# Kernel optimization log

Measured on AMD Instinct MI355X. Metric: run time of the kernel, lower is better.

The kernel has to match this reference:

```python
import jax, jax.numpy as jnp
import numpy as np

N_QUBITS = 8
N_CYCLES = 4
N_LAYERS = 2  # log2(8) - 1
B = 65536

CNOT = jnp.array([[1, 0, 0, 0],
                  [0, 1, 0, 0],
                  [0, 0, 0, 1],
                  [0, 0, 1, 0]], dtype=jnp.complex64)


def apply_gate(state, U, wires):
    """Apply a (2^k x 2^k) gate U on the given wires of state (B, 2,2,...,2).
    Wire 0 is the leftmost (most significant) qubit axis."""
    k = len(wires)
    src = [w + 1 for w in wires]
    dst = list(range(1, 1 + k))
    st = jnp.moveaxis(state, src, dst)
    shp = st.shape
    st = st.reshape(shp[0], 2 ** k, -1)
    st = jnp.einsum('ij,bjr->bir', U, st)
    return jnp.moveaxis(st.reshape(shp), dst, src)


def apply_ry(state, q, angles):
    """Batched RY(angle) on qubit q; angles has shape (B,)."""
    st = jnp.moveaxis(state, q + 1, 1)  # (B, 2, rest...)
    c = jnp.cos(0.5 * angles).reshape((-1,) + (1,) * (st.ndim - 2))
    s = jnp.sin(0.5 * angles).reshape((-1,) + (1,) * (st.ndim - 2))
    s0, s1 = st[:, 0], st[:, 1]
    new = jnp.stack([c * s0 - s * s1, s * s0 + c * s1], axis=1)
    return jnp.moveaxis(new, 1, q + 1)


def crx_mat(theta):
    c = (jnp.cos(0.5 * theta) + 0j).astype(jnp.complex64)
    s = (-1j * jnp.sin(0.5 * theta)).astype(jnp.complex64)
    one = jnp.ones((), jnp.complex64)
    zero = jnp.zeros((), jnp.complex64)
    return jnp.stack([
        jnp.stack([one, zero, zero, zero]),
        jnp.stack([zero, one, zero, zero]),
        jnp.stack([zero, zero, c, s]),
        jnp.stack([zero, zero, s, c]),
    ])


def u3_mat(p):
    th, ph, lm = p[0], p[1], p[2]
    ct = (jnp.cos(0.5 * th) + 0j).astype(jnp.complex64)
    st = (jnp.sin(0.5 * th) + 0j).astype(jnp.complex64)
    el = jnp.exp(1j * lm).astype(jnp.complex64)
    ep = jnp.exp(1j * ph).astype(jnp.complex64)
    return jnp.stack([
        jnp.stack([ct, -el * st]),
        jnp.stack([ep * st, ep * el * ct]),
    ])


def expval_z(state, q):
    st = jnp.moveaxis(state, q + 1, 1)
    p = (st.real ** 2 + st.imag ** 2).reshape(st.shape[0], 2, -1).sum(-1)
    return p[:, 0] - p[:, 1]


def _forward(x, crx_theta, u3_params, w1, b1, w2, b2):
    b = x.shape[0]
    # |0...0> initial state, shape (B, 2,2,...,2)
    state = jnp.zeros((b, 2 ** N_QUBITS), jnp.complex64).at[:, 0].set(1.0)
    state = state.reshape((b,) + (2,) * N_QUBITS)
    # encoder: data re-uploading RY angle encoding + CNOT ring, n_cycles times
    for _ in range(N_CYCLES):
        for q in range(N_QUBITS):
            state = apply_ry(state, q, x[:, q])
        for q in range(N_QUBITS):
            state = apply_gate(state, CNOT, [q, (q + 1) % N_QUBITS])
    # QCNN conv/pool layers with shared weights per layer
    active = list(range(N_QUBITS))
    for layer in range(N_LAYERS):
        U = crx_mat(crx_theta[layer])
        for i in range(0, len(active) - 1, 2):
            state = apply_gate(state, U, [active[i], active[i + 1]])
        for i in range(1, len(active) - 1, 2):
            state = apply_gate(state, U, [active[i], active[i + 1]])
        remain = active[1::2]
        # mid-circuit expval in the original is discarded and does not alter state
        V = u3_mat(u3_params[layer])
        for q in remain:
            state = apply_gate(state, V, [q])
        active = remain
    feats = jnp.stack([expval_z(state, q) for q in active], axis=1)  # (B, 2)
    h = jnp.tanh(feats @ w1 + b1)
    return jax.nn.sigmoid(h @ w2 + b2)  # (B, 1)


def setup_inputs() -> dict:
    key = jax.random.key(0)
    ks = jax.random.split(key, 6)
    return {
        'x': jax.random.normal(ks[0], (B, N_QUBITS), jnp.float32),
        'crx_theta': jax.random.normal(ks[1], (N_LAYERS,), jnp.float32),
        'u3_params': jax.random.normal(ks[2], (N_LAYERS, 3), jnp.float32),
        'w1': jax.random.normal(ks[3], (2, 10), jnp.float32) * 0.5,
        'b1': jnp.zeros((10,), jnp.float32),
        'w2': jax.random.normal(ks[4], (10, 1), jnp.float32) * 0.5,
        'b2': jnp.zeros((1,), jnp.float32),
    }


def reference(x, crx_theta, u3_params, w1, b1, w2, b2):
    return _forward(x, crx_theta, u3_params, w1, b1, w2, b2)
```

## Files before the change

kernel.cpp:

```cpp
#include <hip/hip_runtime.h>


#define NQ 8
#define NE 2
#define FRAG_OFF 0
#define UR_OFF   65536
#define UI_OFF   98304

typedef _Float16 h2 __attribute__((ext_vector_type(2)));
typedef _Float16 h8 __attribute__((ext_vector_type(8)));
typedef float    f4 __attribute__((ext_vector_type(4)));

__device__ __forceinline__ float h2f(h2 v){ return __builtin_bit_cast(float, v); }
__device__ __forceinline__ h2 f2h(float v){ return __builtin_bit_cast(h2, v); }
__device__ __forceinline__ h2 u2h(unsigned u){ return __builtin_bit_cast(h2, u); }
__device__ __forceinline__ unsigned h2u(h2 v){ return __builtin_bit_cast(unsigned, v); }
__device__ __forceinline__ h2 negh(h2 v){ return u2h(h2u(v) ^ 0x80008000u); }
__device__ __forceinline__ h2 mk(float x){ return __builtin_bit_cast(h2, __builtin_amdgcn_cvt_pkrtz(x,x)); }
__device__ __forceinline__ h2 mk2(float a, float b){ return __builtin_bit_cast(h2, __builtin_amdgcn_cvt_pkrtz(a,b)); }
__device__ __forceinline__ h2 fma2h(h2 a, h2 b, h2 c){ return __builtin_elementwise_fma(a,b,c); }
__device__ __forceinline__ h2 swp(h2 v){ return __builtin_shufflevector(v,v,1,0); }

template<int CTRL>
__device__ __forceinline__ float dppf(float v){
    return __int_as_float(__builtin_amdgcn_mov_dpp(__float_as_int(v), CTRL, 0xF, 0xF, true));
}
template<int M>
__device__ __forceinline__ float sx(float v){
    if constexpr (M==1)       return dppf<0xB1>(v);
    else if constexpr (M==2)  return dppf<0x4E>(v);
    else if constexpr (M==32) return __shfl_xor(v, 32, 64);
    else return __int_as_float(__builtin_amdgcn_ds_swizzle(__float_as_int(v), (M<<10)|0x1F));
}
__device__ __forceinline__ void cmulh(h2&R, h2&I, h2 C, h2 S, h2 nS){
    h2 nR = fma2h(C, R, nS*I);
    I = fma2h(C, I, S*R);
    R = nR;
}

#define FOR_E _Pragma("unroll") for (int e = 0; e < NE; ++e)

#define RINGF() do { FOR_E { \
    h2 TA = pb ? B[e] : A[e]; \
    h2 TS = pb ? A[e] : B[e]; \
    int V0 = (int)__builtin_amdgcn_perm(h2u(TS), h2u(TA), 0x07060100u); \
    int V1 = (int)__builtin_amdgcn_perm(h2u(TA), h2u(TS), 0x07060100u); \
    unsigned r0 = (unsigned)__builtin_amdgcn_ds_bpermute(ba0, V0); \
    unsigned r1 = (unsigned)__builtin_amdgcn_ds_bpermute(ba1, V1); \
    A[e] = u2h(__builtin_amdgcn_perm(r1, r0, 0x07060100u)); \
    B[e] = u2h(__builtin_amdgcn_perm(r1, r0, 0x05040302u)); } \
} while(0)

struct P2C {
    h2 cc0,sn0,nsn0, cc1,sn1,nsn1;
    h2 uct0,ust0,nust0,usv0;
    h2 uct1,ust1,nust1;
    h2 cl1,sl1,nsl1, cp1,sp1,nsp1;
    h2 E0,E1,E2,E3,G2,G3;
    h2 Clm,Slm,nSlm,Cph,Sph,nSph;
    h2 tu1,tu3,tu5;
};

__device__ __forceinline__ P2C load_consts(const unsigned* wsu, int l){
    P2C K;
    const bool L4=(l>>4)&1, L2=(l>>2)&1, L0=l&1;
    K.cc0=u2h(wsu[0]); K.sn0=u2h(wsu[1]); K.cc1=u2h(wsu[2]); K.sn1=u2h(wsu[3]);
    K.nsn0=negh(K.sn0); K.nsn1=negh(K.sn1);
    K.uct0=u2h(wsu[4]); K.ust0=u2h(wsu[5]); K.nust0=u2h(wsu[6]); K.usv0=u2h(wsu[7]);
    K.uct1=u2h(wsu[8]); K.ust1=u2h(wsu[9]); K.nust1=u2h(wsu[10]);
    K.cl1=u2h(wsu[11]); K.sl1=u2h(wsu[12]); K.nsl1=negh(K.sl1);
    K.cp1=u2h(wsu[13]); K.sp1=u2h(wsu[14]); K.nsp1=negh(K.sp1);
    K.E0=u2h(wsu[15]); K.E1=u2h(wsu[16]); K.E2=u2h(wsu[17]);
    K.E3=u2h(wsu[18]); K.G2=u2h(wsu[19]); K.G3=u2h(wsu[20]);
    const int ki = (int)L4 + (int)L2 + (int)L0;
    K.Clm=u2h(wsu[24+ki*4+0]); K.Slm=u2h(wsu[24+ki*4+1]);
    K.Cph=u2h(wsu[24+ki*4+2]); K.Sph=u2h(wsu[24+ki*4+3]);
    K.nSlm=negh(K.Slm); K.nSph=negh(K.Sph);
    K.tu1 = L4 ? K.ust0 : K.nust0;
    K.tu3 = L2 ? K.ust0 : K.nust0;
    K.tu5 = L0 ? K.ust0 : K.nust0;
    return K;
}

#define SHF4(M) h2 oRA[NE], oIA[NE], oRB[NE], oIB[NE]; \
    FOR_E { oRA[e]=f2h(sx<M>(h2f(RA[e]))); oIA[e]=f2h(sx<M>(h2f(IA[e]))); \
            oRB[e]=f2h(sx<M>(h2f(RB[e]))); oIB[e]=f2h(sx<M>(h2f(IB[e]))); }
#define CRX_LL(CSH, M, cc, sn, nsn) do { \
    const bool ct = (l >> (CSH)) & 1; \
    SHF4(M) \
    if (ct) { FOR_E { \
        RA[e] = fma2h(cc, RA[e], (sn)*oIA[e]); IA[e] = fma2h(cc, IA[e], (nsn)*oRA[e]); \
        RB[e] = fma2h(cc, RB[e], (sn)*oIB[e]); IB[e] = fma2h(cc, IB[e], (nsn)*oRB[e]); } } \
} while(0)
#define RYC0(M, T) do { \
    SHF4(M) \
    FOR_E { \
    RA[e] = fma2h(K.uct0, RA[e], (T)*oRA[e]); IA[e] = fma2h(K.uct0, IA[e], (T)*oIA[e]); \
    RB[e] = fma2h(K.uct0, RB[e], (T)*oRB[e]); IB[e] = fma2h(K.uct0, IB[e], (T)*oIB[e]); } \
} while(0)

__device__ __forceinline__ void phase2run(const int l, const P2C& K,
    const h2* A, const h2* B, h2* RA, h2* RB, h2* IA, h2* IB)
{
    const bool L5=(l>>5)&1, L2=(l>>2)&1, L0=l&1;
    FOR_E { RA[e]=A[e]; RB[e]=B[e]; IA[e]=(h2){0,0}; IB[e]=(h2){0,0}; }

    {   h2 oA[NE], oB[NE];
        FOR_E { oA[e]=f2h(sx<16>(h2f(RA[e]))); oB[e]=f2h(sx<16>(h2f(RB[e]))); }
        if (L5){ FOR_E {
            IA[e] = K.nsn0*oA[e]; RA[e] = K.cc0*RA[e];
            IB[e] = K.nsn0*oB[e]; RB[e] = K.cc0*RB[e]; } }
    }
    CRX_LL(3, 4, K.cc0, K.sn0, K.nsn0);
    CRX_LL(1, 1, K.cc0, K.sn0, K.nsn0);
    FOR_E {
        h2 oI = swp(IB[e]), oR = swp(RB[e]);
        RB[e] = fma2h(K.cc0, RB[e], K.sn0*oI);
        IB[e] = fma2h(K.cc0, IB[e], K.nsn0*oR);
    }
    CRX_LL(4, 8, K.cc0, K.sn0, K.nsn0);
    CRX_LL(2, 2, K.cc0, K.sn0, K.nsn0);
    if (L0) { FOR_E {
        h2 nRA = fma2h(K.cc0, RA[e], K.sn0*IB[e]);
        h2 nRB = fma2h(K.cc0, RB[e], K.sn0*IA[e]);
        h2 nIA = fma2h(K.cc0, IA[e], K.nsn0*RB[e]);
        h2 nIB = fma2h(K.cc0, IB[e], K.nsn0*RA[e]);
        RA[e]=nRA; RB[e]=nRB; IA[e]=nIA; IB[e]=nIB; } }
    FOR_E { cmulh(RA[e],IA[e],K.Clm,K.Slm,K.nSlm); cmulh(RB[e],IB[e],K.Clm,K.Slm,K.nSlm); }
    RYC0(16, K.tu1);
    RYC0(4,  K.tu3);
    RYC0(1,  K.tu5);
    FOR_E {
        h2 sA=swp(RA[e]), sB=swp(RB[e]), tA=swp(IA[e]), tB=swp(IB[e]);
        RA[e] = fma2h(K.uct0, RA[e], K.usv0*sA); RB[e] = fma2h(K.uct0, RB[e], K.usv0*sB);
        IA[e] = fma2h(K.uct0, IA[e], K.usv0*tA); IB[e] = fma2h(K.uct0, IB[e], K.usv0*tB);
    }
    FOR_E { cmulh(RA[e],IA[e],K.Cph,K.Sph,K.nSph); cmulh(RB[e],IB[e],K.Cph,K.Sph,K.nSph); }

    CRX_LL(4, 4, K.cc1, K.sn1, K.nsn1);
    if (L0) { FOR_E {
        h2 sIA=swp(IA[e]), sRA=swp(RA[e]), sIB=swp(IB[e]), sRB=swp(RB[e]);
        RA[e] = fma2h(K.cc1, RA[e], K.sn1*sIA); IA[e] = fma2h(K.cc1, IA[e], K.nsn1*sRA);
        RB[e] = fma2h(K.cc1, RB[e], K.sn1*sIB); IB[e] = fma2h(K.cc1, IB[e], K.nsn1*sRB); } }
    CRX_LL(2, 1, K.cc1, K.sn1, K.nsn1);
    {
        if (L2){ FOR_E { cmulh(RA[e],IA[e],K.cl1,K.sl1,K.nsl1); cmulh(RB[e],IB[e],K.cl1,K.sl1,K.nsl1); } }
        h2 T = L2 ? K.ust1 : K.nust1;
        SHF4(4)
        FOR_E {
            RA[e] = fma2h(K.uct1, RA[e], T*oRA[e]); IA[e] = fma2h(K.uct1, IA[e], T*oIA[e]);
            RB[e] = fma2h(K.uct1, RB[e], T*oRB[e]); IB[e] = fma2h(K.uct1, IB[e], T*oIB[e]);
        }
        if (L2){ FOR_E { cmulh(RA[e],IA[e],K.cp1,K.sp1,K.nsp1); cmulh(RB[e],IB[e],K.cp1,K.sp1,K.nsp1); } }
    }
    FOR_E {
        h2 sR=swp(RA[e]), sI=swp(IA[e]);
        h2 nR = fma2h(K.E3,sI, fma2h(K.E2,IA[e], fma2h(K.E1,sR, K.E0*RA[e])));
        h2 nI = fma2h(K.G3,sR, fma2h(K.G2,RA[e], fma2h(K.E1,sI, K.E0*IA[e])));
        RA[e]=nR; IA[e]=nI;
        h2 sR2=swp(RB[e]), sI2=swp(IB[e]);
        h2 nR2 = fma2h(K.E3,sI2, fma2h(K.E2,IB[e], fma2h(K.E1,sR2, K.E0*RB[e])));
        h2 nI2 = fma2h(K.G3,sR2, fma2h(K.G2,RB[e], fma2h(K.E1,sI2, K.E0*IB[e])));
        RB[e]=nR2; IB[e]=nI2;
    }
}

__global__ __launch_bounds__(1024) void qcnn_prep_u(
    const float* __restrict__ crx, const float* __restrict__ u3p,
    unsigned* __restrict__ ws)
{
    __shared__ unsigned cws[48];
    if (threadIdx.x == 0){
        auto PK=[](float lo, float hi)->unsigned{
            unsigned a=__builtin_bit_cast(unsigned short,(_Float16)lo);
            unsigned b=__builtin_bit_cast(unsigned short,(_Float16)hi);
            return a | (b<<16);
        };
        float sc0,cc0,sc1,cc1;
        __sincosf(0.5f*crx[0],&sc0,&cc0);
        __sincosf(0.5f*crx[1],&sc1,&cc1);
        cws[0]=PK(cc0,cc0); cws[1]=PK(sc0,sc0); cws[2]=PK(cc1,cc1); cws[3]=PK(sc1,sc1);
        float th0=u3p[0], ph0=u3p[1], lm0=u3p[2];
        float ust0,uct0; __sincosf(0.5f*th0,&ust0,&uct0);
        cws[4]=PK(uct0,uct0); cws[5]=PK(ust0,ust0); cws[6]=PK(-ust0,-ust0); cws[7]=PK(-ust0,ust0);
        float th1=u3p[3], ph1=u3p[4], lm1=u3p[5];
        float ust1,uct1; __sincosf(0.5f*th1,&ust1,&uct1);
        float sl1,cl1;   __sincosf(lm1,&sl1,&cl1);
        float sp1,cp1;   __sincosf(ph1,&sp1,&cp1);
        cws[8]=PK(uct1,uct1); cws[9]=PK(ust1,ust1); cws[10]=PK(-ust1,-ust1);
        cws[11]=PK(cl1,cl1); cws[12]=PK(sl1,sl1); cws[13]=PK(cp1,cp1); cws[14]=PK(sp1,sp1);
        float cpl1=cp1*cl1-sp1*sl1, spl1=sp1*cl1+cp1*sl1;
        float u01r=-ust1*cl1, u01i=-ust1*sl1;
        float u10r= ust1*cp1, u10i= ust1*sp1;
        float u11r= uct1*cpl1, u11i= uct1*spl1;
        cws[15]=PK(uct1,u11r); cws[16]=PK(u01r,u10r); cws[17]=PK(0.f,-u11i);
        cws[18]=PK(-u01i,-u10i); cws[19]=PK(0.f,u11i); cws[20]=PK(u01i,u10i);
        for(int k=0;k<4;++k){
            float kf=(float)k, sA,cA,sB,cB,sA2,cA2,sB2,cB2;
            __sincosf(lm0*kf,      &sA,&cA);
            __sincosf(lm0*(kf+1.f),&sB,&cB);
            __sincosf(ph0*kf,      &sA2,&cA2);
            __sincosf(ph0*(kf+1.f),&sB2,&cB2);
            unsigned* q = cws + 24 + k*4;
            q[0]=PK(cA,cB); q[1]=PK(sA,sB); q[2]=PK(cA2,cB2); q[3]=PK(sA2,sB2);
        }
    }
    __syncthreads();

    const int l = threadIdx.x & 63;
    const int w = threadIdx.x >> 6;
    const P2C K = load_consts(cws, l);
    const bool pb = __builtin_popcount(l) & 1;
    const int ba0 = (((l&32)|((l^(l>>1))&31)) << 2);
    const int ba1 = ba0 ^ (48<<2);

    const int j0 = blockIdx.x*32 + w*2;
    h2 A[NE], B[NE];
    FOR_E {
        A[e]=(h2){0,0}; B[e]=(h2){0,0};
        const int j = j0 + e;
        if (l == (j >> 2)){
            const int slot = j & 3;
            const _Float16 one = (_Float16)1.f;
            if      (slot==0) A[e].x = one;
            else if (slot==1) A[e].y = one;
            else if (slot==2) B[e].x = one;
            else              B[e].y = one;
        }
    }
    RINGF();
    h2 RA[NE], RB[NE], IA[NE], IB[NE];
    phase2run(l, K, A, B, RA, RB, IA, IB);
    FOR_E {
        const int j = j0 + e;
        *(uint2*)(ws + UR_OFF + j*128 + l*2) = make_uint2(h2u(RA[e]), h2u(RB[e]));
        *(uint2*)(ws + UI_OFF + j*128 + l*2) = make_uint2(h2u(IA[e]), h2u(IB[e]));
    }
}

__global__ void qcnn_prep_frag(unsigned* __restrict__ ws){
    const int T = blockIdx.x*256 + threadIdx.x;
    const int chunk = T >> 6, l = T & 63;
    const int ct = chunk >> 4, ri = (chunk >> 3) & 1, ks = chunk & 7;
    const unsigned short* U = (const unsigned short*)(ws + (ri ? UI_OFF : UR_OFF));
    const int n = ct*16 + (l & 15);
    const int g = l >> 4;
    unsigned d[4];
#pragma unroll
    for (int p = 0; p < 4; ++p){
        const int k0 = ks*32 + g*8 + 2*p;
        unsigned lo = U[k0*256 + n];
        unsigned hi = U[(k0+1)*256 + n];
        d[p] = lo | (hi << 16);
    }
    uint4 v; v.x=d[0]; v.y=d[1]; v.z=d[2]; v.w=d[3];
    *(uint4*)(ws + FRAG_OFF + chunk*256 + l*4) = v;
}

__global__ __launch_bounds__(1024) void qcnn_kernel(
    const float* __restrict__ x,
    const unsigned* __restrict__ wsu,
    const float* __restrict__ w1,
    const float* __restrict__ b1,
    const float* __restrict__ w2,
    const float* __restrict__ b2,
    float* __restrict__ out,
    int Btot)
{
    __shared__ __align__(16) unsigned char Sl[32*1024];
    __shared__ float parts[2][64][17];
    const int tid = threadIdx.x;
    const int l = tid & 63;
    const int w = tid >> 6;
    const int eblk = blockIdx.x * 64;
    const bool L5=(l>>5)&1, L4=(l>>4)&1, L3=(l>>3)&1, L2=(l>>2)&1, L1=(l>>1)&1, L0=l&1;

    const bool pb = __builtin_popcount(l) & 1;
    const int ba0 = (((l&32)|((l^(l>>1))&31)) << 2);
    const int ba1 = ba0 ^ (48<<2);

    const bool bits[6]={L5,L4,L3,L2,L1,L0};
    unsigned sm[6];
#pragma unroll
    for(int q=0;q<6;++q) sm[q] = bits[q] ? 0u : 0x80008000u;

#define RY_L(q, M) do { FOR_E { \
    h2 oA = f2h(sx<M>(h2f(A[e]))), oB = f2h(sx<M>(h2f(B[e]))); \
    A[e] = fma2h(cH[e][q], A[e], tsH[e][q]*oA); \
    B[e] = fma2h(cH[e][q], B[e], tsH[e][q]*oB); } \
} while(0)

#define LADDER() do { \
    RINGF(); \
    _Pragma("unroll") for(int cyc=0;cyc<3;++cyc){ \
        RY_L(0,32); RY_L(1,16); RY_L(2,8); RY_L(3,4); RY_L(4,2); RY_L(5,1); \
        FOR_E { h2 nA = fma2h(c6h[e], A[e], ns6h[e]*B[e]); \
                h2 nB = fma2h(s6h[e], A[e], c6h[e]*B[e]); \
                A[e]=nA; B[e]=nB; } \
        FOR_E { A[e] = fma2h(c7h[e], A[e], sv7h[e]*swp(A[e])); \
                B[e] = fma2h(c7h[e], B[e], sv7h[e]*swp(B[e])); } \
        if (cyc < 2) RINGF(); \
    } \
} while(0)

#define STAGE(rbase) do { FOR_E { \
    const int r = (rbase) + e; \
    const int mblk = r >> 4, rr = r & 15; \
    const int ks = l >> 3, g2 = (l >> 1) & 3, pp = l & 1; \
    const unsigned gran = (unsigned)((rr | (g2<<4)) ^ ks ^ (g2<<1)); \
    const unsigned off = (unsigned)(((mblk*8 + ks) << 10) | (gran << 4) | (pp << 3)); \
    *(uint2*)(Sl + off) = make_uint2(h2u(A[e]), h2u(B[e])); } \
} while(0)

#pragma unroll
    for (int pass = 0; pass < 2; ++pass){
        const int rbase = w*4 + pass*2;
        h2 cH[NE][6], tsH[NE][6];
        h2 c6h[NE], s6h[NE], ns6h[NE], c7h[NE], sv7h[NE];
        h2 A[NE], B[NE];
        FOR_E {
            int ee = eblk + rbase + e; if (ee >= Btot) ee = Btot - 1;
            const float4* xv = (const float4*)(x + ee*NQ);
            float4 xa=xv[0], xb=xv[1];
            float ang[8]={xa.x,xa.y,xa.z,xa.w,xb.x,xb.y,xb.z,xb.w};
            float cq[8], sq[8];
#pragma unroll
            for(int q=0;q<8;++q) __sincosf(0.5f*ang[q], &sq[q], &cq[q]);
#pragma unroll
            for(int q=0;q<6;++q){
                cH[e][q]=mk(cq[q]);
                tsH[e][q]=u2h(h2u(mk(sq[q])) ^ sm[q]);
            }
            c6h[e]=mk(cq[6]); s6h[e]=mk(sq[6]); ns6h[e]=negh(s6h[e]);
            c7h[e]=mk(cq[7]); sv7h[e]=mk2(-sq[7], sq[7]);
            float pl = (L5?sq[0]:cq[0])*(L4?sq[1]:cq[1])*(L3?sq[2]:cq[2])
                     * (L2?sq[3]:cq[3])*(L1?sq[4]:cq[4])*(L0?sq[5]:cq[5]);
            float pc6=pl*cq[6], ps6=pl*sq[6];
            A[e] = mk2(pc6*cq[7], pc6*sq[7]);
            B[e] = mk2(ps6*cq[7], ps6*sq[7]);
        }
        LADDER();
        STAGE(rbase);
    }
    __syncthreads();

    const int g = l >> 4;
    const unsigned* frag = wsu + FRAG_OFF;

#define REDU(aR, aI, mb) do { \
    _Pragma("unroll") for (int r = 0; r < 4; ++r){ \
        float nv = fmaf(aR[r], aR[r], aI[r]*aI[r]); \
        float o  = sx<1>(nv); \
        float v0 = nv + o, v1 = nv - o; \
        v0 += sx<2>(v0); v1 += sx<2>(v1); \
        v0 += sx<4>(v0); v1 += sx<4>(v1); \
        v0 += sx<8>(v0); v1 += sx<8>(v1); \
        if ((l & 15) == 0){ \
            parts[0][(mb)*16 + g*4 + r][w] = v0; \
            parts[1][(mb)*16 + g*4 + r][w] = v1; } \
    } \
} while(0)

#pragma unroll
    for (int half = 0; half < 2; ++half){
        f4 aRa={0,0,0,0}, aIa={0,0,0,0}, aRb={0,0,0,0}, aIb={0,0,0,0};
        const int mb0 = half*2, mb1 = half*2 + 1;
#pragma unroll
        for (int ks = 0; ks < 8; ++ks){
            h8 br = *(const h8*)(frag + (w*16 +     ks)*256 + l*4);
            h8 bi = *(const h8*)(frag + (w*16 + 8 + ks)*256 + l*4);
            const unsigned ga = (unsigned)((l ^ ks ^ (g<<1)) << 4);
            h8 a0 = *(const h8*)(Sl + ((mb0*8 + ks) << 10) + ga);
            h8 a1 = *(const h8*)(Sl + ((mb1*8 + ks) << 10) + ga);
            aRa = __builtin_amdgcn_mfma_f32_16x16x32_f16(a0, br, aRa, 0, 0, 0);
            aIa = __builtin_amdgcn_mfma_f32_16x16x32_f16(a0, bi, aIa, 0, 0, 0);
            aRb = __builtin_amdgcn_mfma_f32_16x16x32_f16(a1, br, aRb, 0, 0, 0);
            aIb = __builtin_amdgcn_mfma_f32_16x16x32_f16(a1, bi, aIb, 0, 0, 0);
        }
        REDU(aRa, aIa, mb0);
        REDU(aRb, aIb, mb1);
    }
    __syncthreads();

    {
        const int elem = tid >> 4, k = tid & 15;
        float F0 = parts[0][elem][k];
        float F1 = parts[1][elem][k];
        F0 = __int_as_float(__float_as_int(F0) ^ ((k & 1) << 31));
        F0 += sx<1>(F0); F0 += sx<2>(F0); F0 += sx<4>(F0); F0 += sx<8>(F0);
        F1 += sx<1>(F1); F1 += sx<2>(F1); F1 += sx<4>(F1); F1 += sx<8>(F1);
        float contrib = 0.0f;
        if (k < 10){
            float z = fmaf(F0, w1[k], fmaf(F1, w1[10+k], b1[k]));
            float ex = __expf(2.0f*z);
            contrib = ((ex-1.0f)/(ex+1.0f)) * w2[k];
        }
        contrib += sx<1>(contrib);
        contrib += sx<2>(contrib);
        contrib += sx<4>(contrib);
        contrib += sx<8>(contrib);
        if (k == 0 && eblk + elem < Btot){
            out[eblk + elem] = 1.0f/(1.0f + __expf(-(contrib + b2[0])));
        }
    }
}

extern "C" void kernel_launch(void* const* d_in, const int* in_sizes, int n_in,
                              void* d_out, int out_size, void* d_ws, size_t ws_size,
                              hipStream_t stream) {
    const float* x   = (const float*)d_in[0];
    const float* crx = (const float*)d_in[1];
    const float* u3p = (const float*)d_in[2];
    const float* w1  = (const float*)d_in[3];
    const float* b1  = (const float*)d_in[4];
    const float* w2  = (const float*)d_in[5];
    const float* b2  = (const float*)d_in[6];
    float* out = (float*)d_out;
    unsigned* ws = (unsigned*)d_ws;

    const int B = in_sizes[0] / NQ;
    hipLaunchKernelGGL(qcnn_prep_u,    dim3(8),  dim3(1024), 0, stream, crx, u3p, ws);
    hipLaunchKernelGGL(qcnn_prep_frag, dim3(64), dim3(256),  0, stream, ws);
    const int grid = (B + 63) / 64;
    hipLaunchKernelGGL(qcnn_kernel, dim3(grid), dim3(1024), 0, stream,
                       x, ws, w1, b1, w2, b2, out, B);
}
```

Measured before the change: 128.6 us.

## Split fused kernel into state-prep kernel and GEMM kernel via workspace

Divides the single fused kernel into two launches. The first runs the per-sample RY/CRX ladder in 256-thread blocks and writes the fp16 state vectors to a workspace region. The second reloads them into swizzled LDS and runs the MFMA unitary GEMM plus the reduction with 512 threads, each wave covering two column tiles. The aim is to decouple the occupancy limits of the two phases, at the cost of an extra global round-trip of 32 MB (read and write) and an extra launch. The old fused kernel is kept as a fallback when the workspace is too small.

```diff
diff --git a/kernel.cpp b/kernel.cpp
--- a/kernel.cpp
+++ b/kernel.cpp
@@ -6,6 +6,7 @@
 #define FRAG_OFF 0
 #define UR_OFF   65536
 #define UI_OFF   98304
+#define SG_OFF   131072
 
 typedef _Float16 h2 __attribute__((ext_vector_type(2)));
 typedef _Float16 h8 __attribute__((ext_vector_type(8)));
@@ -164,6 +165,58 @@
         RB[e]=nR2; IB[e]=nI2;
     }
 }
+
+#define RY_L(q, M) do { FOR_E { \
+    h2 oA = f2h(sx<M>(h2f(A[e]))), oB = f2h(sx<M>(h2f(B[e]))); \
+    A[e] = fma2h(cH[e][q], A[e], tsH[e][q]*oA); \
+    B[e] = fma2h(cH[e][q], B[e], tsH[e][q]*oB); } \
+} while(0)
+
+#define LADDER() do { \
+    RINGF(); \
+    _Pragma("unroll") for(int cyc=0;cyc<3;++cyc){ \
+        RY_L(0,32); RY_L(1,16); RY_L(2,8); RY_L(3,4); RY_L(4,2); RY_L(5,1); \
+        FOR_E { h2 nA = fma2h(c6h[e], A[e], ns6h[e]*B[e]); \
+                h2 nB = fma2h(s6h[e], A[e], c6h[e]*B[e]); \
+                A[e]=nA; B[e]=nB; } \
+        FOR_E { A[e] = fma2h(c7h[e], A[e], sv7h[e]*swp(A[e])); \
+                B[e] = fma2h(c7h[e], B[e], sv7h[e]*swp(B[e])); } \
+        if (cyc < 2) RINGF(); \
+    } \
+} while(0)
+
+#define BUILD_COEF_INLINE(eeexpr) FOR_E { \
+    int ee = (eeexpr); if (ee >= Btot) ee = Btot - 1; \
+    const float4* xv = (const float4*)(x + ee*NQ); \
+    float4 xa=xv[0], xb=xv[1]; \
+    float ang[8]={xa.x,xa.y,xa.z,xa.w,xb.x,xb.y,xb.z,xb.w}; \
+    float cq[8], sq[8]; \
+    _Pragma("unroll") for(int q=0;q<8;++q) __sincosf(0.5f*ang[q], &sq[q], &cq[q]); \
+    _Pragma("unroll") for(int q=0;q<6;++q){ \
+        cH[e][q]=mk(cq[q]); \
+        tsH[e][q]=u2h(h2u(mk(sq[q])) ^ sm[q]); } \
+    c6h[e]=mk(cq[6]); s6h[e]=mk(sq[6]); ns6h[e]=negh(s6h[e]); \
+    c7h[e]=mk(cq[7]); sv7h[e]=mk2(-sq[7], sq[7]); \
+    float pl = (L5?sq[0]:cq[0])*(L4?sq[1]:cq[1])*(L3?sq[2]:cq[2]) \
+             * (L2?sq[3]:cq[3])*(L1?sq[4]:cq[4])*(L0?sq[5]:cq[5]); \
+    float pc6=pl*cq[6], ps6=pl*sq[6]; \
+    A[e] = mk2(pc6*cq[7], pc6*sq[7]); \
+    B[e] = mk2(ps6*cq[7], ps6*sq[7]); \
+}
+
+#define REDU(aR, aI, mb, CT) do { \
+    _Pragma("unroll") for (int r = 0; r < 4; ++r){ \
+        float nv = fmaf(aR[r], aR[r], aI[r]*aI[r]); \
+        float o  = sx<1>(nv); \
+        float v0 = nv + o, v1 = nv - o; \
+        v0 += sx<2>(v0); v1 += sx<2>(v1); \
+        v0 += sx<4>(v0); v1 += sx<4>(v1); \
+        v0 += sx<8>(v0); v1 += sx<8>(v1); \
+        if ((l & 15) == 0){ \
+            parts[0][(mb)*16 + g*4 + r][CT] = v0; \
+            parts[1][(mb)*16 + g*4 + r][CT] = v1; } \
+    } \
+} while(0)
 
 __global__ __launch_bounds__(1024) void qcnn_prep_u(
     const float* __restrict__ crx, const float* __restrict__ u3p,
@@ -257,7 +310,123 @@
     *(uint4*)(ws + FRAG_OFF + chunk*256 + l*4) = v;
 }
 
-__global__ __launch_bounds__(1024) void qcnn_kernel(
+__global__ __launch_bounds__(256) void qcnn_s1(
+    const float* __restrict__ x, unsigned* __restrict__ ws, int Btot)
+{
+    const int gtid = blockIdx.x*256 + threadIdx.x;
+    const int wv = gtid >> 6;
+    const int l = threadIdx.x & 63;
+    const int e0 = wv * NE;
+    if (e0 >= Btot) return;
+    const bool L5=(l>>5)&1, L4=(l>>4)&1, L3=(l>>3)&1, L2=(l>>2)&1, L1=(l>>1)&1, L0=l&1;
+    const bool pb = __builtin_popcount(l) & 1;
+    const int ba0 = (((l&32)|((l^(l>>1))&31)) << 2);
+    const int ba1 = ba0 ^ (48<<2);
+    const bool bits[6]={L5,L4,L3,L2,L1,L0};
+    unsigned sm[6];
+#pragma unroll
+    for(int q=0;q<6;++q) sm[q] = bits[q] ? 0u : 0x80008000u;
+
+    h2 cH[NE][6], tsH[NE][6];
+    h2 c6h[NE], s6h[NE], ns6h[NE], c7h[NE], sv7h[NE];
+    h2 A[NE], B[NE];
+    BUILD_COEF_INLINE(e0 + e);
+    LADDER();
+    FOR_E {
+        const int ee = e0 + e;
+        if (ee < Btot)
+            *(uint2*)(ws + SG_OFF + ee*128 + l*2) = make_uint2(h2u(A[e]), h2u(B[e]));
+    }
+}
+
+__global__ __launch_bounds__(512) void qcnn_gemm(
+    const unsigned* __restrict__ wsu,
+    const float* __restrict__ w1,
+    const float* __restrict__ b1,
+    const float* __restrict__ w2,
+    const float* __restrict__ b2,
+    float* __restrict__ out,
+    int Btot)
+{
+    __shared__ __align__(16) unsigned char Sl[32*1024];
+    __shared__ float parts[2][64][17];
+    const int tid = threadIdx.x;
+    const int l = tid & 63;
+    const int w = tid >> 6;
+    const int eblk = blockIdx.x * 64;
+
+#pragma unroll
+    for (int i = 0; i < 8; ++i){
+        const int idx = tid + i*512;
+        const int r = idx >> 6, ll = idx & 63;
+        int ee = eblk + r; if (ee >= Btot) ee = Btot - 1;
+        uint2 v = *(const uint2*)(wsu + SG_OFF + ee*128 + ll*2);
+        const int mblk = r >> 4, rr = r & 15;
+        const int ks = ll >> 3, g2 = (ll >> 1) & 3, pp = ll & 1;
+        const unsigned gran = (unsigned)((rr | (g2<<4)) ^ ks ^ (g2<<1));
+        const unsigned off = (unsigned)(((mblk*8 + ks) << 10) | (gran << 4) | (pp << 3));
+        *(uint2*)(Sl + off) = v;
+    }
+    __syncthreads();
+
+    const int g = l >> 4;
+    const unsigned* frag = wsu + FRAG_OFF;
+#pragma unroll
+    for (int j = 0; j < 2; ++j){
+        const int ct = w*2 + j;
+        f4 aR0={0,0,0,0}, aI0={0,0,0,0}, aR1={0,0,0,0}, aI1={0,0,0,0};
+        f4 aR2={0,0,0,0}, aI2={0,0,0,0}, aR3={0,0,0,0}, aI3={0,0,0,0};
+#pragma unroll
+        for (int ks = 0; ks < 8; ++ks){
+            h8 br = *(const h8*)(frag + (ct*16 +     ks)*256 + l*4);
+            h8 bi = *(const h8*)(frag + (ct*16 + 8 + ks)*256 + l*4);
+            const unsigned ga = (unsigned)((l ^ ks ^ (g<<1)) << 4);
+            h8 a0 = *(const h8*)(Sl + ((0*8 + ks) << 10) + ga);
+            h8 a1 = *(const h8*)(Sl + ((1*8 + ks) << 10) + ga);
+            h8 a2 = *(const h8*)(Sl + ((2*8 + ks) << 10) + ga);
+            h8 a3 = *(const h8*)(Sl + ((3*8 + ks) << 10) + ga);
+            aR0 = __builtin_amdgcn_mfma_f32_16x16x32_f16(a0, br, aR0, 0, 0, 0);
+            aI0 = __builtin_amdgcn_mfma_f32_16x16x32_f16(a0, bi, aI0, 0, 0, 0);
+            aR1 = __builtin_amdgcn_mfma_f32_16x16x32_f16(a1, br, aR1, 0, 0, 0);
+            aI1 = __builtin_amdgcn_mfma_f32_16x16x32_f16(a1, bi, aI1, 0, 0, 0);
+            aR2 = __builtin_amdgcn_mfma_f32_16x16x32_f16(a2, br, aR2, 0, 0, 0);
+            aI2 = __builtin_amdgcn_mfma_f32_16x16x32_f16(a2, bi, aI2, 0, 0, 0);
+            aR3 = __builtin_amdgcn_mfma_f32_16x16x32_f16(a3, br, aR3, 0, 0, 0);
+            aI3 = __builtin_amdgcn_mfma_f32_16x16x32_f16(a3, bi, aI3, 0, 0, 0);
+        }
+        REDU(aR0, aI0, 0, ct);
+        REDU(aR1, aI1, 1, ct);
+        REDU(aR2, aI2, 2, ct);
+        REDU(aR3, aI3, 3, ct);
+    }
+    __syncthreads();
+
+#pragma unroll
+    for (int half = 0; half < 2; ++half){
+        const int elem = (tid >> 4) + half*32;
+        const int k = tid & 15;
+        float F0 = parts[0][elem][k];
+        float F1 = parts[1][elem][k];
+        F0 = __int_as_float(__float_as_int(F0) ^ ((k & 1) << 31));
+        F0 += sx<1>(F0); F0 += sx<2>(F0); F0 += sx<4>(F0); F0 += sx<8>(F0);
+        F1 += sx<1>(F1); F1 += sx<2>(F1); F1 += sx<4>(F1); F1 += sx<8>(F1);
+        float contrib = 0.0f;
+        if (k < 10){
+            float z = fmaf(F0, w1[k], fmaf(F1, w1[10+k], b1[k]));
+            float ex = __expf(2.0f*z);
+            contrib = ((ex-1.0f)/(ex+1.0f)) * w2[k];
+        }
+        contrib += sx<1>(contrib);
+        contrib += sx<2>(contrib);
+        contrib += sx<4>(contrib);
+        contrib += sx<8>(contrib);
+        if (k == 0 && eblk + elem < Btot){
+            out[eblk + elem] = 1.0f/(1.0f + __expf(-(contrib + b2[0])));
+        }
+    }
+}
+
+__global__ __launch_bounds__(1024) void qcnn_fused(
     const float* __restrict__ x,
     const unsigned* __restrict__ wsu,
     const float* __restrict__ w1,
@@ -274,43 +443,13 @@
     const int w = tid >> 6;
     const int eblk = blockIdx.x * 64;
     const bool L5=(l>>5)&1, L4=(l>>4)&1, L3=(l>>3)&1, L2=(l>>2)&1, L1=(l>>1)&1, L0=l&1;
-
     const bool pb = __builtin_popcount(l) & 1;
     const int ba0 = (((l&32)|((l^(l>>1))&31)) << 2);
     const int ba1 = ba0 ^ (48<<2);
-
     const bool bits[6]={L5,L4,L3,L2,L1,L0};
     unsigned sm[6];
 #pragma unroll
     for(int q=0;q<6;++q) sm[q] = bits[q] ? 0u : 0x80008000u;
-
-#define RY_L(q, M) do { FOR_E { \
-    h2 oA = f2h(sx<M>(h2f(A[e]))), oB = f2h(sx<M>(h2f(B[e]))); \
-    A[e] = fma2h(cH[e][q], A[e], tsH[e][q]*oA); \
-    B[e] = fma2h(cH[e][q], B[e], tsH[e][q]*oB); } \
-} while(0)
-
-#define LADDER() do { \
-    RINGF(); \
-    _Pragma("unroll") for(int cyc=0;cyc<3;++cyc){ \
-        RY_L(0,32); RY_L(1,16); RY_L(2,8); RY_L(3,4); RY_L(4,2); RY_L(5,1); \
-        FOR_E { h2 nA = fma2h(c6h[e], A[e], ns6h[e]*B[e]); \
-                h2 nB = fma2h(s6h[e], A[e], c6h[e]*B[e]); \
-                A[e]=nA; B[e]=nB; } \
-        FOR_E { A[e] = fma2h(c7h[e], A[e], sv7h[e]*swp(A[e])); \
-                B[e] = fma2h(c7h[e], B[e], sv7h[e]*swp(B[e])); } \
-        if (cyc < 2) RINGF(); \
-    } \
-} while(0)
-
-#define STAGE(rbase) do { FOR_E { \
-    const int r = (rbase) + e; \
-    const int mblk = r >> 4, rr = r & 15; \
-    const int ks = l >> 3, g2 = (l >> 1) & 3, pp = l & 1; \
-    const unsigned gran = (unsigned)((rr | (g2<<4)) ^ ks ^ (g2<<1)); \
-    const unsigned off = (unsigned)(((mblk*8 + ks) << 10) | (gran << 4) | (pp << 3)); \
-    *(uint2*)(Sl + off) = make_uint2(h2u(A[e]), h2u(B[e])); } \
-} while(0)
 
 #pragma unroll
     for (int pass = 0; pass < 2; ++pass){
@@ -318,49 +457,21 @@
         h2 cH[NE][6], tsH[NE][6];
         h2 c6h[NE], s6h[NE], ns6h[NE], c7h[NE], sv7h[NE];
         h2 A[NE], B[NE];
+        BUILD_COEF_INLINE(eblk + rbase + e);
+        LADDER();
         FOR_E {
-            int ee = eblk + rbase + e; if (ee >= Btot) ee = Btot - 1;
-            const float4* xv = (const float4*)(x + ee*NQ);
-            float4 xa=xv[0], xb=xv[1];
-            float ang[8]={xa.x,xa.y,xa.z,xa.w,xb.x,xb.y,xb.z,xb.w};
-            float cq[8], sq[8];
-#pragma unroll
-            for(int q=0;q<8;++q) __sincosf(0.5f*ang[q], &sq[q], &cq[q]);
-#pragma unroll
-            for(int q=0;q<6;++q){
-                cH[e][q]=mk(cq[q]);
-                tsH[e][q]=u2h(h2u(mk(sq[q])) ^ sm[q]);
-            }
-            c6h[e]=mk(cq[6]); s6h[e]=mk(sq[6]); ns6h[e]=negh(s6h[e]);
-            c7h[e]=mk(cq[7]); sv7h[e]=mk2(-sq[7], sq[7]);
-            float pl = (L5?sq[0]:cq[0])*(L4?sq[1]:cq[1])*(L3?sq[2]:cq[2])
-                     * (L2?sq[3]:cq[3])*(L1?sq[4]:cq[4])*(L0?sq[5]:cq[5]);
-            float pc6=pl*cq[6], ps6=pl*sq[6];
-            A[e] = mk2(pc6*cq[7], pc6*sq[7]);
-            B[e] = mk2(ps6*cq[7], ps6*sq[7]);
-        }
-        LADDER();
-        STAGE(rbase);
+            const int r = rbase + e;
+            const int mblk = r >> 4, rr = r & 15;
+            const int ks = l >> 3, g2 = (l >> 1) & 3, pp = l & 1;
+            const unsigned gran = (unsigned)((rr | (g2<<4)) ^ ks ^ (g2<<1));
+            const unsigned off = (unsigned)(((mblk*8 + ks) << 10) | (gran << 4) | (pp << 3));
+            *(uint2*)(Sl + off) = make_uint2(h2u(A[e]), h2u(B[e]));
+        }
     }
     __syncthreads();
 
     const int g = l >> 4;
     const unsigned* frag = wsu + FRAG_OFF;
-
-#define REDU(aR, aI, mb) do { \
-    _Pragma("unroll") for (int r = 0; r < 4; ++r){ \
-        float nv = fmaf(aR[r], aR[r], aI[r]*aI[r]); \
-        float o  = sx<1>(nv); \
-        float v0 = nv + o, v1 = nv - o; \
-        v0 += sx<2>(v0); v1 += sx<2>(v1); \
-        v0 += sx<4>(v0); v1 += sx<4>(v1); \
-        v0 += sx<8>(v0); v1 += sx<8>(v1); \
-        if ((l & 15) == 0){ \
-            parts[0][(mb)*16 + g*4 + r][w] = v0; \
-            parts[1][(mb)*16 + g*4 + r][w] = v1; } \
-    } \
-} while(0)
-
 #pragma unroll
     for (int half = 0; half < 2; ++half){
         f4 aRa={0,0,0,0}, aIa={0,0,0,0}, aRb={0,0,0,0}, aIb={0,0,0,0};
@@ -377,8 +488,8 @@
             aRb = __builtin_amdgcn_mfma_f32_16x16x32_f16(a1, br, aRb, 0, 0, 0);
             aIb = __builtin_amdgcn_mfma_f32_16x16x32_f16(a1, bi, aIb, 0, 0, 0);
         }
-        REDU(aRa, aIa, mb0);
-        REDU(aRb, aIb, mb1);
+        REDU(aRa, aIa, mb0, w);
+        REDU(aRb, aIb, mb1, w);
     }
     __syncthreads();
 
@@ -421,7 +532,15 @@
     const int B = in_sizes[0] / NQ;
     hipLaunchKernelGGL(qcnn_prep_u,    dim3(8),  dim3(1024), 0, stream, crx, u3p, ws);
     hipLaunchKernelGGL(qcnn_prep_frag, dim3(64), dim3(256),  0, stream, ws);
-    const int grid = (B + 63) / 64;
-    hipLaunchKernelGGL(qcnn_kernel, dim3(grid), dim3(1024), 0, stream,
-                       x, ws, w1, b1, w2, b2, out, B);
-}
+
+    const size_t need = ((size_t)SG_OFF + (size_t)B * 128) * 4;
+    if (ws_size >= need) {
+        hipLaunchKernelGGL(qcnn_s1, dim3((B + 7) / 8), dim3(256), 0, stream,
+                           x, ws, B);
+        hipLaunchKernelGGL(qcnn_gemm, dim3((B + 63) / 64), dim3(512), 0, stream,
+                           ws, w1, b1, w2, b2, out, B);
+    } else {
+        hipLaunchKernelGGL(qcnn_fused, dim3((B + 63) / 64), dim3(1024), 0, stream,
+                           x, ws, w1, b1, w2, b2, out, B);
+    }
+}
```

Result: slower. 142.3 us (+10.7%).
